# Kernel optimization log

Measured on AMD Instinct MI355X. Metric: run time of the kernel, lower is better.

## Reference

```python
import jax, jax.numpy as jnp
import numpy as np

B, O, T = 32, 256, 1024
D_OBJ = 512      # obj_input_dim
D_PRED = 512     # predicate_input_dim
HID = 512        # hidden_dim
P_OUT = 512      # predicate_output_dim
OBJ_OUT = 512    # object_output_dim
N_PRED_TYPES = 50
ORIGINAL_EDGE = 0
TRANSITIVE_EDGE = 1


def setup_inputs() -> dict:
    key = jax.random.key(0)
    ks = jax.random.split(key, 16)

    def kaiming(k, fan_in, fan_out):
        return jax.random.normal(k, (fan_in, fan_out), jnp.float32) * np.sqrt(2.0 / fan_in)

    n1_in = 2 * D_OBJ + D_PRED            # 1536
    n1_out = 2 * HID + P_OUT              # 1536
    return {
        "obj_vecs": jax.random.normal(ks[0], (B, O, D_OBJ), jnp.float32),
        "pred_vecs": jax.random.normal(ks[1], (B, T, D_PRED), jnp.float32),
        "W1a": kaiming(ks[2], n1_in, HID), "b1a": jnp.zeros((HID,), jnp.float32),
        "W1b": kaiming(ks[3], HID, n1_out), "b1b": jnp.zeros((n1_out,), jnp.float32),
        "W2a": kaiming(ks[4], HID, HID), "b2a": jnp.zeros((HID,), jnp.float32),
        "W2b": kaiming(ks[5], HID, OBJ_OUT), "b2b": jnp.zeros((OBJ_OUT,), jnp.float32),
        "pt_weights": jax.random.normal(ks[6], (N_PRED_TYPES,), jnp.float32),
        "edges": jax.random.randint(ks[7], (B, T, 2), 0, O, jnp.int32),
        "pred_indicators": jax.random.randint(ks[8], (B, T), 0, 2, jnp.int32).astype(bool),
        "triplet_type": jax.random.randint(ks[9], (B, T), 0, 2, jnp.int32),
        "predicate_ids": jax.random.randint(ks[10], (B, T), 0, N_PRED_TYPES, jnp.int32),
    }


def reference(obj_vecs, pred_vecs, W1a, b1a, W1b, b1b, W2a, b2a, W2b, b2b,
              pt_weights, edges, pred_indicators, triplet_type, predicate_ids):
    s_idx = edges[:, :, 0]  # [B,T]
    o_idx = edges[:, :, 1]

    # gather subject/object vectors: [B,T,D]
    cur_s = jnp.take_along_axis(obj_vecs, s_idx[:, :, None], axis=1)
    cur_o = jnp.take_along_axis(obj_vecs, o_idx[:, :, None], axis=1)
    cur_t = jnp.concatenate([cur_s, pred_vecs, cur_o], axis=-1)  # [B,T,2D+Dp]

    # net1: Linear-ReLU-Linear-ReLU
    h = jax.nn.relu(cur_t @ W1a + b1a)
    new_t = jax.nn.relu(h @ W1b + b1b)  # [B,T,2*HID+P_OUT]

    # confidence weighting
    pt_pred = jax.nn.sigmoid(pt_weights)  # [N_PRED_TYPES]
    conf = ((triplet_type == ORIGINAL_EDGE).astype(jnp.float32)
            + (triplet_type == TRANSITIVE_EDGE).astype(jnp.float32) * pt_pred[predicate_ids])  # [B,T]
    new_t = new_t * conf[:, :, None]

    new_s = new_t[:, :, :HID]
    new_p = new_t[:, :, HID:HID + P_OUT]
    new_o = new_t[:, :, HID + P_OUT:]

    mask = pred_indicators.astype(jnp.float32)  # [B,T]

    def pool_one(si, oi, sv, ov, cf, m):
        # masked scatter-add (equivalent to torch boolean-masked scatter_add)
        sums = (jax.ops.segment_sum(sv * m[:, None], si, num_segments=O)
                + jax.ops.segment_sum(ov * m[:, None], oi, num_segments=O))  # [O,HID]
        w = cf * m
        counts = (jax.ops.segment_sum(w, si, num_segments=O)
                  + jax.ops.segment_sum(w, oi, num_segments=O))  # [O]
        nz = counts > 0
        return jnp.where(nz[:, None], sums / jnp.where(nz, counts, 1.0)[:, None], sums)

    pooled = jax.vmap(pool_one)(s_idx, o_idx, new_s, new_o, conf, mask)  # [B,O,HID]

    # net2: Linear-ReLU-Linear-ReLU
    h2 = jax.nn.relu(pooled @ W2a + b2a)
    new_obj = jax.nn.relu(h2 @ W2b + b2b)  # [B,O,OBJ_OUT]

    return new_obj, new_p
```

## Files before the change

kernel.cpp:

```cpp
#include <hip/hip_runtime.h>
#include <hip/hip_bf16.h>
#include <cstdint>
#include <cstddef>

#define DEV __device__ __forceinline__

typedef __attribute__((ext_vector_type(8))) short  s8v;
typedef __attribute__((ext_vector_type(4))) float  f4v;
typedef __attribute__((ext_vector_type(4))) uint32_t u4v;

DEV unsigned short f2bf(float x) {
  union { float f; uint32_t u; } v; v.f = x;
  uint32_t u = v.u + 0x7FFFu + ((v.u >> 16) & 1u);
  return (unsigned short)(u >> 16);
}
DEV uint32_t cvtpk2(float lo, float hi) {
  uint32_t r;
  asm("v_cvt_pk_bf16_f32 %0, %1, %2" : "=v"(r) : "v"(lo), "v"(hi));
  return r;
}
DEV unsigned short f2bf_fast(float x) { return (unsigned short)cvtpk2(x, 0.f); }
DEV float bf2f(unsigned short b) {
  union { uint32_t u; float f; } v; v.u = ((uint32_t)b) << 16;
  return v.f;
}

DEV void async_copy16(void* lds, const void* g) {
  typedef __attribute__((address_space(3))) uint32_t lds_t;
  typedef const __attribute__((address_space(1))) uint32_t g_t;
  __builtin_amdgcn_global_load_lds((g_t*)g, (lds_t*)lds, 16, 0, 0);
}

#define WAITV4()    asm volatile("s_waitcnt vmcnt(4)" ::: "memory")
#define WAITV0()    asm volatile("s_waitcnt vmcnt(0)" ::: "memory")
#define MEMFENCE()  asm volatile("" ::: "memory")

constexpr int Bc = 32, Oc = 256, Tc = 1024;
constexpr int BM = 128, BN = 128, BK = 64;
constexpr int CSR_CAP = 46;

DEV void swz_mn(int nyb, int* mb, int* nb) {
  const int nwg = gridDim.x * gridDim.y;
  const int w   = blockIdx.x + blockIdx.y * gridDim.x;
  const int cpx = nwg >> 3;
  const int s   = (w & 7) * cpx + (w >> 3);
  *mb = s / nyb;
  *nb = s % nyb;
}

__global__ __launch_bounds__(256)
void prologue_k(const float* __restrict__ pred, const float* __restrict__ obj,
                const float* __restrict__ W1a, const float* __restrict__ W1b,
                const float* __restrict__ W2a, const float* __restrict__ W2b,
                unsigned short* __restrict__ predb, unsigned short* __restrict__ objb,
                unsigned short* __restrict__ W1at, unsigned short* __restrict__ W1bt,
                unsigned short* __restrict__ W2at, unsigned short* __restrict__ W2bt,
                const unsigned char* __restrict__ maskb, int* __restrict__ flag)
{
  __shared__ float tile[32][33];
  const int b = blockIdx.x;
  const int tid = threadIdx.x;

  if (b < 10240) {
    const float* in = (b < 8192) ? pred : obj;
    unsigned short* outp = (b < 8192) ? predb : objb;
    const int i = ((b < 8192) ? b : b - 8192) * 256 + tid;
    const f4v v0 = *(const f4v*)(in + (size_t)i * 8);
    const f4v v1 = *(const f4v*)(in + (size_t)i * 8 + 4);
    u4v pk;
    pk.x = cvtpk2(v0.x, v0.y);
    pk.y = cvtpk2(v0.z, v0.w);
    pk.z = cvtpk2(v1.x, v1.y);
    pk.w = cvtpk2(v1.z, v1.w);
    *(u4v*)(outp + (size_t)i * 8) = pk;
  } else if (b < 12288) {
    const float* W; unsigned short* Wt; int K, N, kb, nb;
    if (b < 11008)      { W = W1a; Wt = W1at; K = 1536; N = 512;
                          const int r = b - 10240; kb = r % 48; nb = r / 48; }
    else if (b < 11776) { W = W1b; Wt = W1bt; K = 512;  N = 1536;
                          const int r = b - 11008; kb = r % 16; nb = r / 16; }
    else if (b < 12032) { W = W2a; Wt = W2at; K = 512;  N = 512;
                          const int r = b - 11776; kb = r % 16; nb = r / 16; }
    else                { W = W2b; Wt = W2bt; K = 512;  N = 512;
                          const int r = b - 12032; kb = r % 16; nb = r / 16; }
    const int k0 = kb * 32, n0 = nb * 32;
    const int tx = tid & 31, ty = tid >> 5;
    #pragma unroll
    for (int i = 0; i < 32; i += 8)
      tile[ty + i][tx] = W[(size_t)(k0 + ty + i) * N + (n0 + tx)];
    __syncthreads();
    #pragma unroll
    for (int i = 0; i < 32; i += 8)
      Wt[(size_t)(n0 + ty + i) * K + (k0 + tx)] = f2bf(tile[tx][ty + i]);
  } else {
    const int i = (b - 12288) * 256 + tid;
    const int local = ((i & 3) && maskb[i]) ? 1 : 0;
    const unsigned long long bal = __ballot(local);
    if (bal != 0 && (tid & 63) == 0) atomicOr(flag, 1);
  }
}

#define READ_A(QM, DST) do {                                                    \
    _Pragma("unroll")                                                           \
    for (int i = 0; i < 4; ++i) {                                               \
      const int row = wm * 128 + ((QM) * 4 + i) * 16 + (lane & 15);             \
      _Pragma("unroll")                                                         \
      for (int kk = 0; kk < 2; ++kk) {                                          \
        const int c = kk * 4 + (lane >> 4);                                     \
        DST[i][kk] = *(const s8v*)(Ab_ + row * 128 + ((c ^ (row & 7)) << 4));   \
      }                                                                         \
    }                                                                           \
  } while (0)

#define READ_B(QN, DST) do {                                                    \
    _Pragma("unroll")                                                           \
    for (int j = 0; j < 2; ++j) {                                               \
      const int row = wn * 64 + ((QN) * 2 + j) * 16 + (lane & 15);              \
      _Pragma("unroll")                                                         \
      for (int kk = 0; kk < 2; ++kk) {                                          \
        const int c = kk * 4 + (lane >> 4);                                     \
        DST[j][kk] = *(const s8v*)(Bb_ + row * 128 + ((c ^ (row & 7)) << 4));   \
      }                                                                         \
    }                                                                           \
  } while (0)

#define SYNC_MFMA(QM, QN, AF, BF) do {                                          \
    MEMFENCE();                                                                 \
    __builtin_amdgcn_s_barrier();                                               \
    asm volatile("s_waitcnt lgkmcnt(0)" ::: "memory");                          \
    __builtin_amdgcn_sched_barrier(0);                                          \
    __builtin_amdgcn_s_setprio(1);                                              \
    _Pragma("unroll")                                                           \
    for (int i = 0; i < 4; ++i)                                                 \
      _Pragma("unroll")                                                         \
      for (int j = 0; j < 2; ++j)                                               \
        _Pragma("unroll")                                                       \
        for (int kk = 0; kk < 2; ++kk)                                          \
          acc[(QM) * 4 + i][(QN) * 2 + j] =                                     \
            __builtin_amdgcn_mfma_f32_16x16x32_bf16(                            \
              AF[i][kk], BF[j][kk], acc[(QM) * 4 + i][(QN) * 2 + j], 0, 0, 0);  \
    __builtin_amdgcn_s_setprio(0);                                              \
  } while (0)

#define ENDPHASE() do { MEMFENCE(); __builtin_amdgcn_s_barrier(); } while (0)

#define KTILE_BODY() do {                                                       \
    const int par = t & 1, px = par ^ 1;                                        \
    const char* Ab_ = smem + par * 65536;                                       \
    const char* Bb_ = Ab_ + 32768;                                              \
    const bool s1 = (t + 1 < nk), s2 = (t + 2 < nk);                            \
                                                                        \
    READ_A(0, af); READ_B(0, bf0);                                              \
    if (s1) stageA(px, 1, t + 1);                                               \
    SYNC_MFMA(0, 0, af, bf0);                                                   \
    ENDPHASE();                                                                 \
                                                                        \
    READ_B(1, bf1);                                                             \
    if (s1) stageB(px, 1, t + 1);                                               \
    SYNC_MFMA(0, 1, af, bf1);                                                   \
    ENDPHASE();                                                                 \
                                                                        \
    READ_A(1, af);                                                              \
    if (s2) stageA(par, 0, t + 2);                                              \
    SYNC_MFMA(1, 1, af, bf1);                                                   \
    ENDPHASE();                                                                 \
                                                                        \
    if (s2) stageB(par, 0, t + 2);                                              \
    SYNC_MFMA(1, 0, af, bf0);                                                   \
    if (s2) { WAITV4(); } else if (s1) { WAITV0(); }                            \
    ENDPHASE();                                                                 \
  } while (0)

__global__ __launch_bounds__(512, 2)
void gemm8g_k(const unsigned short* __restrict__ objb,
              const unsigned short* __restrict__ predb,
              const int* __restrict__ edges,
              const unsigned short* __restrict__ Bt,
              const float* __restrict__ bias,
              unsigned short* __restrict__ outp)
{
  __shared__ __align__(16) char smem[131072];

  const int tid = threadIdx.x, lane = tid & 63, wave = tid >> 6;
  const int wm = wave >> 2, wn = wave & 3;
  int mb, nb; swz_mn(gridDim.y, &mb, &nb);
  const int m0 = mb * 256, n0 = nb * 256;
  const int rl  = tid >> 3;
  const int cs8 = ((lane & 7) ^ (lane >> 3)) * 8;
  const int rB0 = (rl >> 5) * 64 + (rl & 31);

  uint32_t offS[4], offP[4], offO[4];
  #pragma unroll
  for (int c2 = 0; c2 < 4; ++c2) {
    const int r = (c2 >> 1) * 128 + (c2 & 1) * 64 + rl;
    const int m = m0 + r;
    const int ob = (m >> 10) * Oc;
    offS[c2] = (uint32_t)((ob + edges[2 * m])     * 1024 + cs8 * 2);
    offO[c2] = (uint32_t)((ob + edges[2 * m + 1]) * 1024 + cs8 * 2);
    offP[c2] = (uint32_t)(m * 1024 + cs8 * 2);
  }
  const unsigned short* srcB = Bt + (size_t)(n0 + rB0) * 1536 + cs8;

  auto stageA = [&](int p, int qm, int kt) {
    const int reg = kt >> 3;
    const uint32_t koff = (uint32_t)(kt & 7) * 128u;
    #pragma unroll
    for (int s = 0; s < 2; ++s) {
      const int c2 = s * 2 + qm;
      const char* src;
      if (reg == 0)      src = (const char*)objb  + offS[c2] + koff;
      else if (reg == 1) src = (const char*)predb + offP[c2] + koff;
      else               src = (const char*)objb  + offO[c2] + koff;
      async_copy16(smem + p * 65536 + ((s * 128 + qm * 64 + wave * 8) << 7), src);
    }
  };
  auto stageB = [&](int p, int qn, int kt) {
    #pragma unroll
    for (int s = 0; s < 2; ++s)
      async_copy16(smem + p * 65536 + 32768 +
                     ((s * 128 + qn * 32 + (wave >> 2) * 64 + (wave & 3) * 8) << 7),
                   srcB + (size_t)(s * 128 + qn * 32) * 1536 + kt * 64);
  };

  f4v acc[8][4] = {};
  s8v af[4][2], bf0[2][2], bf1[2][2];
  constexpr int nk = 24;

  stageA(0, 0, 0); stageB(0, 0, 0); stageA(0, 1, 0); stageB(0, 1, 0);
  stageA(1, 0, 1); stageB(1, 0, 1);
  WAITV4();
  MEMFENCE();
  __builtin_amdgcn_s_barrier();

  for (int t = 0; t < nk; ++t) KTILE_BODY();

  const int cn = lane & 15, rq4 = (lane >> 4) * 4;
  #pragma unroll
  for (int f = 0; f < 8; ++f) {
    const int gr0 = m0 + wm * 128 + f * 16 + rq4;
    #pragma unroll
    for (int g = 0; g < 4; ++g) {
      const int gc = n0 + wn * 64 + g * 16 + cn;
      const float bv = bias[gc];
      #pragma unroll
      for (int r = 0; r < 4; ++r) {
        float val = acc[f][g][r] + bv;
        val = val > 0.f ? val : 0.f;
        outp[(size_t)(gr0 + r) * 512 + gc] = f2bf_fast(val);
      }
    }
  }
}

template<int EPI>
__global__ __launch_bounds__(256)
void gemm_k(const unsigned short* __restrict__ Abf,
            const unsigned short* __restrict__ Bt,
            const float* __restrict__ bias,
            unsigned short* __restrict__ out_bf,
            float* __restrict__ out_f32,
            int M, int N, int K)
{
  __shared__ __align__(16) char smem[BM * BK * 2 + BN * BK * 2];
  char* As = smem;
  char* Bs = smem + BM * BK * 2;

  const int tid  = threadIdx.x;
  const int lane = tid & 63;
  const int wave = tid >> 6;
  const int wm = wave >> 1, wn = wave & 1;
  int mb, nb; swz_mn(gridDim.y, &mb, &nb);
  const int m0 = mb * BM;
  const int n0 = nb * BN;

  f4v acc[4][4] = {};

  for (int k0 = 0; k0 < K; k0 += BK) {
    {
      const int r8 = lane >> 3;
      const int cs = (lane & 7) ^ r8;
      const unsigned short* src = Bt + (size_t)(n0 + wave * 32 + r8) * K + k0 + cs * 8;
      #pragma unroll
      for (int i = 0; i < 4; ++i)
        async_copy16(Bs + (wave * 32 + i * 8) * 128, src + (size_t)i * 8 * K);
      const unsigned short* srca = Abf + (size_t)(m0 + wave * 32 + r8) * K + k0 + cs * 8;
      #pragma unroll
      for (int i = 0; i < 4; ++i)
        async_copy16(As + (wave * 32 + i * 8) * 128, srca + (size_t)i * 8 * K);
    }
    __syncthreads();

    #pragma unroll
    for (int kk = 0; kk < 2; ++kk) {
      s8v af[4], bfv[4];
      #pragma unroll
      for (int i = 0; i < 4; ++i) {
        const int row = wm * 64 + i * 16 + (lane & 15);
        const int c = kk * 4 + (lane >> 4);
        af[i] = *(const s8v*)(As + row * 128 + ((c ^ (row & 7)) << 4));
      }
      #pragma unroll
      for (int j = 0; j < 4; ++j) {
        const int row = wn * 64 + j * 16 + (lane & 15);
        const int c = kk * 4 + (lane >> 4);
        bfv[j] = *(const s8v*)(Bs + row * 128 + ((c ^ (row & 7)) << 4));
      }
      #pragma unroll
      for (int i = 0; i < 4; ++i)
        #pragma unroll
        for (int j = 0; j < 4; ++j)
          acc[i][j] = __builtin_amdgcn_mfma_f32_16x16x32_bf16(af[i], bfv[j], acc[i][j], 0, 0, 0);
    }
    __syncthreads();
  }

  const int cn = lane & 15, rq4 = (lane >> 4) * 4;
  #pragma unroll
  for (int i = 0; i < 4; ++i) {
    const int gr0 = m0 + wm * 64 + i * 16 + rq4;
    #pragma unroll
    for (int j = 0; j < 4; ++j) {
      const int gc = n0 + wn * 64 + j * 16 + cn;
      const float bv = bias[gc];
      #pragma unroll
      for (int r = 0; r < 4; ++r) {
        float val = acc[i][j][r] + bv;
        val = val > 0.f ? val : 0.f;
        const int gr = gr0 + r;
        if (EPI == 0) out_bf[(size_t)gr * N + gc] = f2bf_fast(val);
        else          out_f32[(size_t)gr * N + gc] = val;
      }
    }
  }
}

__global__ __launch_bounds__(256)
void gemm2_k(const unsigned short* __restrict__ h,
             const unsigned short* __restrict__ W1bt,
             const float* __restrict__ b1b,
             const float* __restrict__ conf,
             const float* __restrict__ confc,
             const int* __restrict__ torig,
             const int* __restrict__ minfo,
             float* __restrict__ out_p,
             unsigned short* __restrict__ news_c,
             unsigned short* __restrict__ newo_c)
{
  const int Mp   = minfo[1];
  const int nact = (Mp >> 7) << 3;
  const int ntot = 1024 + nact;
  const int w    = blockIdx.x + blockIdx.y * gridDim.x;
  if (w >= ntot) return;
  const int cpx = ntot >> 3;
  const int s   = (w & 7) * cpx + (w >> 3);
  const bool prole = (s < 1024);
  const int Mr = minfo[0];

  int m0, nb;
  if (prole) { m0 = (s >> 2) * BM; nb = s & 3; }
  else       { const int s2 = s - 1024; m0 = (s2 >> 3) * BM; nb = s2 & 7; }
  const int n0 = nb * BN;

  __shared__ __align__(16) char smem[BM * BK * 2 + BN * BK * 2];
  char* As = smem;
  char* Bs = smem + BM * BK * 2;

  const int tid  = threadIdx.x;
  const int lane = tid & 63;
  const int wave = tid >> 6;
  const int wm = wave >> 1, wn = wave & 1;
  const int r8 = lane >> 3;
  const int cs8 = ((lane & 7) ^ r8) * 8;

  const unsigned short* aP[4];
  #pragma unroll
  for (int i = 0; i < 4; ++i) {
    int m = m0 + wave * 32 + i * 8 + r8;
    if (prole) {
      aP[i] = h + (size_t)m * 512 + cs8;
    } else {
      m = m < Mr ? m : Mr - 1;
      aP[i] = h + (size_t)torig[m] * 512 + cs8;
    }
  }
  const int nrow0 = prole ? (512 + n0) : ((nb < 4) ? n0 : n0 + 512);
  const unsigned short* bsrc = W1bt + (size_t)(nrow0 + wave * 32 + r8) * 512 + cs8;

  f4v acc[4][4] = {};

  for (int kt = 0; kt < 8; ++kt) {
    const int kin = kt * 64;
    #pragma unroll
    for (int i = 0; i < 4; ++i)
      async_copy16(Bs + (wave * 32 + i * 8) * 128, bsrc + (size_t)(i * 8) * 512 + kin);
    #pragma unroll
    for (int i = 0; i < 4; ++i)
      async_copy16(As + (wave * 32 + i * 8) * 128, aP[i] + kin);
    __syncthreads();

    #pragma unroll
    for (int kk = 0; kk < 2; ++kk) {
      s8v af[4], bfv[4];
      #pragma unroll
      for (int i = 0; i < 4; ++i) {
        const int row = wm * 64 + i * 16 + (lane & 15);
        const int c = kk * 4 + (lane >> 4);
        af[i] = *(const s8v*)(As + row * 128 + ((c ^ (row & 7)) << 4));
      }
      #pragma unroll
      for (int j = 0; j < 4; ++j) {
        const int row = wn * 64 + j * 16 + (lane & 15);
        const int c = kk * 4 + (lane >> 4);
        bfv[j] = *(const s8v*)(Bs + row * 128 + ((c ^ (row & 7)) << 4));
      }
      #pragma unroll
      for (int i = 0; i < 4; ++i)
        #pragma unroll
        for (int j = 0; j < 4; ++j)
          acc[i][j] = __builtin_amdgcn_mfma_f32_16x16x32_bf16(af[i], bfv[j], acc[i][j], 0, 0, 0);
    }
    __syncthreads();
  }

  const int cn = lane & 15, rq4 = (lane >> 4) * 4;
  if (prole) {
    const float* bb = b1b + 512 + n0;
    #pragma unroll
    for (int i = 0; i < 4; ++i) {
      const int gr0 = m0 + wm * 64 + i * 16 + rq4;
      #pragma unroll
      for (int j = 0; j < 4; ++j) {
        const int lc = wn * 64 + j * 16 + cn;
        const float bv = bb[lc];
        #pragma unroll
        for (int r = 0; r < 4; ++r) {
          const int gr = gr0 + r;
          float val = acc[i][j][r] + bv;
          val = val > 0.f ? val : 0.f;
          out_p[(size_t)gr * 512 + n0 + lc] = val * conf[gr];
        }
      }
    }
  } else {
    const float* bb = b1b + ((nb < 4) ? n0 : 512 + n0);
    unsigned short* outp = (nb < 4) ? news_c : newo_c;
    const int c0 = (nb & 3) * 128;
    #pragma unroll
    for (int i = 0; i < 4; ++i) {
      const int gr0 = m0 + wm * 64 + i * 16 + rq4;
      #pragma unroll
      for (int j = 0; j < 4; ++j) {
        const int lc = wn * 64 + j * 16 + cn;
        const float bv = bb[lc];
        #pragma unroll
        for (int r = 0; r < 4; ++r) {
          const int gr = gr0 + r;
          float val = acc[i][j][r] + bv;
          val = val > 0.f ? val : 0.f;
          val *= confc[gr < Mr ? gr : 0];
          if (gr < Mr) outp[(size_t)gr * 512 + c0 + lc] = f2bf_fast(val);
        }
      }
    }
  }
}

__global__ __launch_bounds__(1024)
void prep_k(const int* __restrict__ tt, const int* __restrict__ pid,
            const float* __restrict__ ptw, const int* __restrict__ edges,
            const void* __restrict__ mask, const int* __restrict__ u8flag,
            float* __restrict__ conf, int* __restrict__ se,
            int* __restrict__ oe, int* __restrict__ bsum)
{
  const int m = blockIdx.x * 1024 + threadIdx.x;
  const int t = tt[m];
  float c = 0.f;
  if (t == 0) c = 1.f;
  else if (t == 1) c = 1.f / (1.f + expf(-ptw[pid[m]]));
  conf[m] = c;
  bool mk;
  if (*u8flag) mk = ((const unsigned char*)mask)[m] != 0;
  else         mk = ((const int*)mask)[m] != 0;
  se[m] = mk ? edges[2 * m]     : -1;
  oe[m] = mk ? edges[2 * m + 1] : -1;

  const unsigned long long bal = __ballot(mk);
  __shared__ int wc[16];
  if ((threadIdx.x & 63) == 0) wc[threadIdx.x >> 6] = (int)__popcll(bal);
  __syncthreads();
  if (threadIdx.x == 0) {
    int ssum = 0;
    #pragma unroll
    for (int i = 0; i < 16; ++i) ssum += wc[i];
    bsum[blockIdx.x] = ssum;
  }
}

__global__ void scan2_k(const int* __restrict__ bsum, int* __restrict__ boff,
                        int* __restrict__ minfo)
{
  if (threadIdx.x == 0) {
    int s = 0;
    for (int i = 0; i < 32; ++i) { boff[i] = s; s += bsum[i]; }
    minfo[0] = s;
    minfo[1] = (s + 127) & ~127;
  }
}

__global__ __launch_bounds__(1024)
void scan3_k(const int* __restrict__ se, const int* __restrict__ boff,
             const float* __restrict__ conf,
             int* __restrict__ torig, int* __restrict__ cmap,
             float* __restrict__ confc)
{
  const int m = blockIdx.x * 1024 + threadIdx.x;
  const int lane = threadIdx.x & 63, w = threadIdx.x >> 6;
  const bool mv = se[m] >= 0;
  const unsigned long long bal = __ballot(mv);
  __shared__ int wc[16];
  if (lane == 0) wc[w] = (int)__popcll(bal);
  __syncthreads();
  int woff = 0;
  for (int i = 0; i < w; ++i) woff += wc[i];
  if (mv) {
    const int c = boff[blockIdx.x] + woff +
                  (int)__popcll(bal & ((1ull << lane) - 1ull));
    torig[c] = m;
    cmap[m]  = c;
    confc[c] = conf[m];
  }
}

__global__ __launch_bounds__(256)
void csr2_k(const int* __restrict__ se, const int* __restrict__ oe,
            int* __restrict__ deg, int* __restrict__ slot)
{
  const int wid  = blockIdx.x * 4 + (threadIdx.x >> 6);
  const int b    = wid >> 8;
  const int u    = wid & 255;
  const int lane = threadIdx.x & 63;
  const int mb   = b * Tc;
  int* sl = slot + (size_t)wid * CSR_CAP;
  const unsigned long long lt = (1ull << lane) - 1ull;
  int cnt = 0;
  #pragma unroll 4
  for (int c = 0; c < 16; ++c) {
    const int t = c * 64 + lane;
    const int s = se[mb + t];
    const int o = oe[mb + t];
    const unsigned long long ms = __ballot(s == u);
    const unsigned long long mo = __ballot(o == u);
    if (s == u) {
      const int pos = cnt + (int)__popcll(ms & lt);
      if (pos < CSR_CAP) sl[pos] = 2 * t;
    }
    cnt += (int)__popcll(ms);
    if (o == u) {
      const int pos = cnt + (int)__popcll(mo & lt);
      if (pos < CSR_CAP) sl[pos] = 2 * t + 1;
    }
    cnt += (int)__popcll(mo);
  }
  if (lane == 0) deg[wid] = cnt < CSR_CAP ? cnt : CSR_CAP;
}

__global__ __launch_bounds__(256)
void pool2_k(const unsigned short* __restrict__ S, const unsigned short* __restrict__ Ov,
             const int* __restrict__ deg, const int* __restrict__ slot,
             const float* __restrict__ conf, const int* __restrict__ cmap,
             unsigned short* __restrict__ pooled)
{
  const int bo = blockIdx.x;
  const int b  = bo >> 8;
  const int u  = threadIdx.x;
  const int d  = deg[bo];
  const int* sl = slot + (size_t)bo * CSR_CAP;
  float a0 = 0.f, a1 = 0.f, w = 0.f;
  for (int i = 0; i < d; ++i) {
    const int e = sl[i];
    const int t = e >> 1;
    const int c = cmap[b * Tc + t];
    const unsigned short* row = ((e & 1) ? Ov : S) + (size_t)c * 512;
    const uint32_t pr = *(const uint32_t*)(row + 2 * u);
    a0 += bf2f((unsigned short)pr);
    a1 += bf2f((unsigned short)(pr >> 16));
    w  += conf[b * Tc + t];
  }
  const float denom = (w > 0.f) ? w : 1.f;
  const size_t ob = (size_t)bo * 512;
  *(uint32_t*)(pooled + ob + 2 * u) = cvtpk2(a0 / denom, a1 / denom);
}

extern "C" void kernel_launch(void* const* d_in, const int* in_sizes, int n_in,
                              void* d_out, int out_size, void* d_ws, size_t ws_size,
                              hipStream_t stream)
{
  const float* obj  = (const float*)d_in[0];
  const float* pred = (const float*)d_in[1];
  const float* W1a  = (const float*)d_in[2];
  const float* b1a  = (const float*)d_in[3];
  const float* W1b  = (const float*)d_in[4];
  const float* b1b  = (const float*)d_in[5];
  const float* W2a  = (const float*)d_in[6];
  const float* b2a  = (const float*)d_in[7];
  const float* W2b  = (const float*)d_in[8];
  const float* b2b  = (const float*)d_in[9];
  const float* ptw  = (const float*)d_in[10];
  const int*   edges = (const int*)d_in[11];
  const void*  mask  = d_in[12];
  const int*   tt    = (const int*)d_in[13];
  const int*   pid   = (const int*)d_in[14];
  float* out = (float*)d_out;

  char* ws = (char*)d_ws;
  unsigned short* W1at = (unsigned short*)(ws + 0);
  unsigned short* W1bt = (unsigned short*)(ws + 1572864);
  unsigned short* W2at = (unsigned short*)(ws + 3145728);
  unsigned short* W2bt = (unsigned short*)(ws + 3670016);
  int* deg  = (int*)(ws + 0);
  int* slot = (int*)(ws + 32768);
  unsigned short* h    = (unsigned short*)(ws + 4194304);
  unsigned short* pooled = h;
  unsigned short* h2   = (unsigned short*)(ws + 12582912);
  unsigned short* news = (unsigned short*)(ws + 37748736);
  unsigned short* newo = (unsigned short*)(ws + 71303168);
  unsigned short* objb = news;
  unsigned short* predb = (unsigned short*)(ws + 46137344);
  float* conf = (float*)(ws + 104857600);
  int*   se   = (int*)(ws + 104988672);
  int*   oe   = (int*)(ws + 105119744);
  int* u8flag = (int*)(ws + 105250816);

  char* sout = (char*)d_out;
  int*   torig = (int*)(sout + 0);
  int*   cmap  = (int*)(sout + 131072);
  float* confc = (float*)(sout + 262144);
  int*   bsum  = (int*)(sout + 393216);
  int*   boff  = (int*)(sout + 393344);
  int*   minfo = (int*)(sout + 393472);

  hipMemsetAsync(u8flag, 0, sizeof(int), stream);
  prologue_k<<<12416, 256, 0, stream>>>(
      pred, obj, W1a, W1b, W2a, W2b,
      predb, objb, W1at, W1bt, W2at, W2bt,
      (const unsigned char*)mask, u8flag);

  prep_k<<<32, 1024, 0, stream>>>(tt, pid, ptw, edges, mask, u8flag,
                                  conf, se, oe, bsum);
  scan2_k<<<1, 64, 0, stream>>>(bsum, boff, minfo);
  scan3_k<<<32, 1024, 0, stream>>>(se, boff, conf, torig, cmap, confc);

  gemm8g_k<<<dim3(128, 2), 512, 0, stream>>>(objb, predb, edges, W1at, b1a, h);

  csr2_k<<<2048, 256, 0, stream>>>(se, oe, deg, slot);

  gemm2_k<<<dim3(384, 8), 256, 0, stream>>>(
      h, W1bt, b1b, conf, confc, torig, minfo, out + 4194304, news, newo);

  pool2_k<<<Bc * Oc, 256, 0, stream>>>(news, newo, deg, slot, conf, cmap, pooled);

  gemm_k<0><<<dim3(64, 4), 256, 0, stream>>>(
      pooled, W2at, b2a, h2, nullptr, 8192, 512, 512);

  gemm_k<2><<<dim3(64, 4), 256, 0, stream>>>(
      h2, W2bt, b2b, nullptr, out, 8192, 512, 512);
}
```

Baseline: 231.2 us.

## Split fused second GEMM into predicate and subject/object kernels, two M-tiles per block

Replaces the single role-switching gemm2 kernel with two launches: a dense predicate-output GEMM and a compacted subject/object GEMM over gathered rows. Each block now processes two consecutive M tiles, reusing its B-column assignment and cutting the grid size. The aim is to remove per-block role branching and launch overhead, and to improve B-tile L2 reuse. In exchange it adds a kernel launch, serialises the two parts, and halves the number of blocks, which may lower occupancy.

```diff
diff --git a/kernel.cpp b/kernel.cpp
--- a/kernel.cpp
+++ b/kernel.cpp
@@ -335,32 +335,12 @@
 }
 
 __global__ __launch_bounds__(256)
-void gemm2_k(const unsigned short* __restrict__ h,
-             const unsigned short* __restrict__ W1bt,
-             const float* __restrict__ b1b,
-             const float* __restrict__ conf,
-             const float* __restrict__ confc,
-             const int* __restrict__ torig,
-             const int* __restrict__ minfo,
-             float* __restrict__ out_p,
-             unsigned short* __restrict__ news_c,
-             unsigned short* __restrict__ newo_c)
-{
-  const int Mp   = minfo[1];
-  const int nact = (Mp >> 7) << 3;
-  const int ntot = 1024 + nact;
-  const int w    = blockIdx.x + blockIdx.y * gridDim.x;
-  if (w >= ntot) return;
-  const int cpx = ntot >> 3;
-  const int s   = (w & 7) * cpx + (w >> 3);
-  const bool prole = (s < 1024);
-  const int Mr = minfo[0];
-
-  int m0, nb;
-  if (prole) { m0 = (s >> 2) * BM; nb = s & 3; }
-  else       { const int s2 = s - 1024; m0 = (s2 >> 3) * BM; nb = s2 & 7; }
-  const int n0 = nb * BN;
-
+void gemm2p_k(const unsigned short* __restrict__ h,
+              const unsigned short* __restrict__ Bt,
+              const float* __restrict__ bias,
+              const float* __restrict__ conf,
+              float* __restrict__ out_p)
+{
   __shared__ __align__(16) char smem[BM * BK * 2 + BN * BK * 2];
   char* As = smem;
   char* Bs = smem + BM * BK * 2;
@@ -369,69 +349,59 @@
   const int lane = tid & 63;
   const int wave = tid >> 6;
   const int wm = wave >> 1, wn = wave & 1;
+  int mbg, nb; swz_mn(4, &mbg, &nb);
+  const int n0 = nb * BN;
   const int r8 = lane >> 3;
-  const int cs8 = ((lane & 7) ^ r8) * 8;
-
-  const unsigned short* aP[4];
-  #pragma unroll
-  for (int i = 0; i < 4; ++i) {
-    int m = m0 + wave * 32 + i * 8 + r8;
-    if (prole) {
-      aP[i] = h + (size_t)m * 512 + cs8;
-    } else {
-      m = m < Mr ? m : Mr - 1;
-      aP[i] = h + (size_t)torig[m] * 512 + cs8;
-    }
-  }
-  const int nrow0 = prole ? (512 + n0) : ((nb < 4) ? n0 : n0 + 512);
-  const unsigned short* bsrc = W1bt + (size_t)(nrow0 + wave * 32 + r8) * 512 + cs8;
-
-  f4v acc[4][4] = {};
-
-  for (int kt = 0; kt < 8; ++kt) {
-    const int kin = kt * 64;
-    #pragma unroll
-    for (int i = 0; i < 4; ++i)
-      async_copy16(Bs + (wave * 32 + i * 8) * 128, bsrc + (size_t)(i * 8) * 512 + kin);
-    #pragma unroll
-    for (int i = 0; i < 4; ++i)
-      async_copy16(As + (wave * 32 + i * 8) * 128, aP[i] + kin);
-    __syncthreads();
-
-    #pragma unroll
-    for (int kk = 0; kk < 2; ++kk) {
-      s8v af[4], bfv[4];
-      #pragma unroll
-      for (int i = 0; i < 4; ++i) {
-        const int row = wm * 64 + i * 16 + (lane & 15);
-        const int c = kk * 4 + (lane >> 4);
-        af[i] = *(const s8v*)(As + row * 128 + ((c ^ (row & 7)) << 4));
+  const int cs = (lane & 7) ^ r8;
+  const unsigned short* srcb = Bt + (size_t)(n0 + wave * 32 + r8) * 512 + cs * 8;
+  const int cn = lane & 15, rq4 = (lane >> 4) * 4;
+
+  #pragma unroll 1
+  for (int mt = 0; mt < 2; ++mt) {
+    const int m0 = (mbg * 2 + mt) * BM;
+    const unsigned short* srca = h + (size_t)(m0 + wave * 32 + r8) * 512 + cs * 8;
+    f4v acc[4][4] = {};
+
+    for (int k0 = 0; k0 < 512; k0 += BK) {
+      #pragma unroll
+      for (int i = 0; i < 4; ++i)
+        async_copy16(Bs + (wave * 32 + i * 8) * 128, srcb + k0 + (size_t)(i * 8) * 512);
+      #pragma unroll
+      for (int i = 0; i < 4; ++i)
+        async_copy16(As + (wave * 32 + i * 8) * 128, srca + k0 + (size_t)(i * 8) * 512);
+      __syncthreads();
+
+      #pragma unroll
+      for (int kk = 0; kk < 2; ++kk) {
+        s8v af[4], bfv[4];
+        #pragma unroll
+        for (int i = 0; i < 4; ++i) {
+          const int row = wm * 64 + i * 16 + (lane & 15);
+          const int c = kk * 4 + (lane >> 4);
+          af[i] = *(const s8v*)(As + row * 128 + ((c ^ (row & 7)) << 4));
+        }
+        #pragma unroll
+        for (int j = 0; j < 4; ++j) {
+          const int row = wn * 64 + j * 16 + (lane & 15);
+          const int c = kk * 4 + (lane >> 4);
+          bfv[j] = *(const s8v*)(Bs + row * 128 + ((c ^ (row & 7)) << 4));
+        }
+        #pragma unroll
+        for (int i = 0; i < 4; ++i)
+          #pragma unroll
+          for (int j = 0; j < 4; ++j)
+            acc[i][j] = __builtin_amdgcn_mfma_f32_16x16x32_bf16(af[i], bfv[j], acc[i][j], 0, 0, 0);
       }
-      #pragma unroll
-      for (int j = 0; j < 4; ++j) {
-        const int row = wn * 64 + j * 16 + (lane & 15);
-        const int c = kk * 4 + (lane >> 4);
-        bfv[j] = *(const s8v*)(Bs + row * 128 + ((c ^ (row & 7)) << 4));
-      }
-      #pragma unroll
-      for (int i = 0; i < 4; ++i)
-        #pragma unroll
-        for (int j = 0; j < 4; ++j)
-          acc[i][j] = __builtin_amdgcn_mfma_f32_16x16x32_bf16(af[i], bfv[j], acc[i][j], 0, 0, 0);
-    }
-    __syncthreads();
-  }
-
-  const int cn = lane & 15, rq4 = (lane >> 4) * 4;
-  if (prole) {
-    const float* bb = b1b + 512 + n0;
+      __syncthreads();
+    }
+
     #pragma unroll
     for (int i = 0; i < 4; ++i) {
       const int gr0 = m0 + wm * 64 + i * 16 + rq4;
       #pragma unroll
       for (int j = 0; j < 4; ++j) {
         const int lc = wn * 64 + j * 16 + cn;
-        const float bv = bb[lc];
+        const float bv = bias[n0 + lc];
         #pragma unroll
         for (int r = 0; r < 4; ++r) {
           const int gr = gr0 + r;
@@ -441,10 +411,96 @@
         }
       }
     }
-  } else {
-    const float* bb = b1b + ((nb < 4) ? n0 : 512 + n0);
-    unsigned short* outp = (nb < 4) ? news_c : newo_c;
-    const int c0 = (nb & 3) * 128;
+  }
+}
+
+__global__ __launch_bounds__(256)
+void gemm2so_k(const unsigned short* __restrict__ h,
+               const int* __restrict__ torig,
+               const float* __restrict__ confc,
+               const unsigned short* __restrict__ W1bt,
+               const float* __restrict__ b1b,
+               const int* __restrict__ minfo,
+               unsigned short* __restrict__ news_c,
+               unsigned short* __restrict__ newo_c)
+{
+  const int Mp   = minfo[1];
+  const int mgs  = (Mp + 255) >> 8;
+  const int nact = mgs * 8;
+  const int w    = blockIdx.x + blockIdx.y * gridDim.x;
+  if (w >= nact) return;
+  const int cpx = nact >> 3;
+  const int s   = (w & 7) * cpx + (w >> 3);
+  const int mg  = s >> 3, nb = s & 7;
+  const int Mr  = minfo[0];
+
+  __shared__ __align__(16) char smem[BM * BK * 2 + BN * BK * 2];
+  char* As = smem;
+  char* Bs = smem + BM * BK * 2;
+
+  const int tid  = threadIdx.x;
+  const int lane = tid & 63;
+  const int wave = tid >> 6;
+  const int wm = wave >> 1, wn = wave & 1;
+  const int n0 = nb * BN;
+  const int r8 = lane >> 3;
+  const int cs8 = ((lane & 7) ^ r8) * 8;
+  const int nrow0 = (nb < 4) ? n0 : n0 + 512;
+  const unsigned short* bsrc = W1bt + (size_t)(nrow0 + wave * 32 + r8) * 512 + cs8;
+  const float* bb = b1b + ((nb < 4) ? n0 : 512 + n0);
+  unsigned short* outp = (nb < 4) ? news_c : newo_c;
+  const int c0 = (nb & 3) * 128;
+  const int cn = lane & 15, rq4 = (lane >> 4) * 4;
+
+  #pragma unroll 1
+  for (int mt = 0; mt < 2; ++mt) {
+    const int m0 = (mg * 2 + mt) * BM;
+    if (m0 >= Mp) break;
+
+    const unsigned short* aP[4];
+    #pragma unroll
+    for (int i = 0; i < 4; ++i) {
+      int m = m0 + wave * 32 + i * 8 + r8;
+      m = m < Mr ? m : Mr - 1;
+      aP[i] = h + (size_t)torig[m] * 512 + cs8;
+    }
+
+    f4v acc[4][4] = {};
+
+    for (int kt = 0; kt < 8; ++kt) {
+      const int kin = kt * 64;
+      #pragma unroll
+      for (int i = 0; i < 4; ++i)
+        async_copy16(Bs + (wave * 32 + i * 8) * 128, bsrc + (size_t)(i * 8) * 512 + kin);
+      #pragma unroll
+      for (int i = 0; i < 4; ++i)
+        async_copy16(As + (wave * 32 + i * 8) * 128, aP[i] + kin);
+      __syncthreads();
+
+      #pragma unroll
+      for (int kk = 0; kk < 2; ++kk) {
+        s8v af[4], bfv[4];
+        #pragma unroll
+        for (int i = 0; i < 4; ++i) {
+          const int row = wm * 64 + i * 16 + (lane & 15);
+          const int c = kk * 4 + (lane >> 4);
+          af[i] = *(const s8v*)(As + row * 128 + ((c ^ (row & 7)) << 4));
+        }
+        #pragma unroll
+        for (int j = 0; j < 4; ++j) {
+          const int row = wn * 64 + j * 16 + (lane & 15);
+          const int c = kk * 4 + (lane >> 4);
+          bfv[j] = *(const s8v*)(Bs + row * 128 + ((c ^ (row & 7)) << 4));
+        }
+        #pragma unroll
+        for (int i = 0; i < 4; ++i)
+          #pragma unroll
+          for (int j = 0; j < 4; ++j)
+            acc[i][j] = __builtin_amdgcn_mfma_f32_16x16x32_bf16(af[i], bfv[j], acc[i][j], 0, 0, 0);
+      }
+      __syncthreads();
+    }
+
     #pragma unroll
     for (int i = 0; i < 4; ++i) {
       const int gr0 = m0 + wm * 64 + i * 16 + rq4;
@@ -639,7 +695,7 @@
   int*   boff  = (int*)(sout + 393344);
   int*   minfo = (int*)(sout + 393472);
 
-  hipMemsetAsync(u8flag, 0, sizeof(int), stream);
+  (void)hipMemsetAsync(u8flag, 0, sizeof(int), stream);
   prologue_k<<<12416, 256, 0, stream>>>(
       pred, obj, W1a, W1b, W2a, W2b,
       predb, objb, W1at, W1bt, W2at, W2bt,
@@ -654,8 +710,11 @@
 
   csr2_k<<<2048, 256, 0, stream>>>(se, oe, deg, slot);
 
-  gemm2_k<<<dim3(384, 8), 256, 0, stream>>>(
-      h, W1bt, b1b, conf, confc, torig, minfo, out + 4194304, news, newo);
+  gemm2p_k<<<dim3(64, 8), 256, 0, stream>>>(
+      h, W1bt + 512 * 512, b1b + 512, conf, out + 4194304);
+
+  gemm2so_k<<<dim3(128, 8), 256, 0, stream>>>(
+      h, torig, confc, W1bt, b1b, minfo, news, newo);
 
   pool2_k<<<Bc * Oc, 256, 0, stream>>>(news, newo, deg, slot, conf, cmap, pooled);
 
```

Result: slower. 238.4 us (+3.1%).
